# Kernel optimization log

Hardware: AMD Instinct MI355X
Metric: run time of the kernel (lower is better)

The kernel has to match this reference:

```python
import jax, jax.numpy as jnp
import numpy as np

N = 100000      # nodes
E = 2000000     # edges
F_NODE = 32     # num_node_features
F_EDGE = 16     # num_edge_features
HID = 128       # size_conv_layers
G = 4096        # num graphs (molecules)
NCLS = 2        # class_weights.shape[0]
NEG = 0.01      # LeakyReLU default negative slope
BN_EPS = 1e-5


def _bn(h, gamma, beta):
    # torch BatchNorm1d training-mode forward: biased batch stats over node dim
    m = jnp.mean(h, axis=0)
    v = jnp.var(h, axis=0)
    return (h - m) * jax.lax.rsqrt(v + BN_EPS) * gamma + beta


def _lrelu(h):
    return jnp.where(h > 0, h, NEG * h)


def setup_inputs() -> dict:
    key = jax.random.key(0)
    ks = jax.random.split(key, 64)
    d = {}
    d["x"] = jax.random.normal(ks[0], (N, F_NODE), dtype=jnp.float32)
    d["edge_index"] = jax.random.randint(ks[1], (2, E), 0, N, dtype=jnp.int64)
    d["edge_attr"] = jax.random.normal(ks[2], (E, F_EDGE), dtype=jnp.float32)
    d["batch"] = jnp.sort(jax.random.randint(ks[3], (N,), 0, G, dtype=jnp.int64))
    dims = [F_NODE, HID, HID]  # in_channels of each conv layer
    i = 4
    for l, ic in enumerate(dims):
        d[f"eps{l}"] = jnp.zeros((), jnp.float32)                                # GINE train_eps init 0
        d[f"ew{l}"] = 0.05 * jax.random.normal(ks[i], (F_EDGE, ic), jnp.float32); i += 1
        d[f"eb{l}"] = jnp.zeros((ic,), jnp.float32)
        d[f"w1{l}"] = 0.05 * jax.random.normal(ks[i], (ic, HID), jnp.float32); i += 1
        d[f"b1{l}"] = jnp.zeros((HID,), jnp.float32)
        d[f"g1{l}"] = jnp.ones((HID,), jnp.float32)
        d[f"be1{l}"] = jnp.zeros((HID,), jnp.float32)
        d[f"w2{l}"] = 0.05 * jax.random.normal(ks[i], (HID, HID), jnp.float32); i += 1
        d[f"b2{l}"] = jnp.zeros((HID,), jnp.float32)
        d[f"g2{l}"] = jnp.ones((HID,), jnp.float32)
        d[f"be2{l}"] = jnp.zeros((HID,), jnp.float32)
    d["wf"] = 0.05 * jax.random.normal(ks[i], (2 * HID, NCLS), jnp.float32)
    d["bf"] = jnp.zeros((NCLS,), jnp.float32)
    return d


def _forward(x, edge_index, edge_attr, batch, layers, wf, bf):
    src = edge_index[0]  # x_j (messages flow source->target in PyG)
    dst = edge_index[1]  # x_i
    for (eps, ew, eb, w1, b1, g1, be1, w2, b2, g2, be2) in layers:
        e = edge_attr @ ew + eb                     # [E, in_ch]
        msg = jax.nn.relu(x[src] + e)               # GINE message
        agg = jax.ops.segment_sum(msg, dst, num_segments=N)
        h = (1.0 + eps) * x + agg                   # [N, in_ch]
        h = _lrelu(_bn(h @ w1 + b1, g1, be1))       # nn: Lin->BN->LeakyReLU
        h = h @ w2 + b2                             # nn: Lin
        x = _lrelu(_bn(h, g2, be2))                 # outer BN + LeakyReLU
    pool = jax.ops.segment_sum(x, batch, num_segments=G)  # global_add_pool
    x_cat = jnp.concatenate([x, pool[batch]], axis=1)      # repeat_interleave broadcast
    logits = x_cat @ wf + bf
    return jax.nn.softmax(logits, axis=1)


def reference(x, edge_index, edge_attr, batch,
              eps0, ew0, eb0, w10, b10, g10, be10, w20, b20, g20, be20,
              eps1, ew1, eb1, w11, b11, g11, be11, w21, b21, g21, be21,
              eps2, ew2, eb2, w12, b12, g12, be12, w22, b22, g22, be22,
              wf, bf):
    layers = [
        (eps0, ew0, eb0, w10, b10, g10, be10, w20, b20, g20, be20),
        (eps1, ew1, eb1, w11, b11, g11, be11, w21, b21, g21, be21),
        (eps2, ew2, eb2, w12, b12, g12, be12, w22, b22, g22, be22),
    ]
    return _forward(x, edge_index, edge_attr, batch, layers, wf, bf)
```

## Files before the change

kernel.cpp:

```cpp
#include <hip/hip_runtime.h>

#define GEMM_GRID 512
#define GNUM 4096

typedef __attribute__((ext_vector_type(8))) short short8_t;
typedef __attribute__((ext_vector_type(4))) float f32x4;

__device__ __forceinline__ float bf2f(unsigned short u) {
    union { unsigned int i; float f; } v; v.i = ((unsigned int)u) << 16; return v.f;
}
__device__ __forceinline__ unsigned short f2bf(float f) {
    union { float f; unsigned int i; } v; v.f = f;
    unsigned int b = v.i + 0x7FFFu + ((v.i >> 16) & 1u);
    return (unsigned short)(b >> 16);
}
__device__ __forceinline__ float lrelu(float v) { return v > 0.f ? v : 0.01f * v; }

__global__ __launch_bounds__(256) void hist_kernel(
    const int* __restrict__ dstv, int* __restrict__ cnt, int E)
{
    int i = blockIdx.x * 256 + threadIdx.x;
    if (i < E) atomicAdd(&cnt[dstv[i] + 1], 1);
}

__global__ __launch_bounds__(256) void scan_block_kernel(
    int* __restrict__ data, int* __restrict__ bsum, int n)
{
    __shared__ int s[256];
    int tid = threadIdx.x;
    int base = blockIdx.x * 1024 + tid * 4;
    int v[4]; int run = 0;
    #pragma unroll
    for (int i = 0; i < 4; i++) {
        int x = (base + i < n) ? data[base + i] : 0;
        run += x; v[i] = run;
    }
    s[tid] = run; __syncthreads();
    for (int off = 1; off < 256; off <<= 1) {
        int t = (tid >= off) ? s[tid - off] : 0;
        __syncthreads();
        s[tid] += t;
        __syncthreads();
    }
    int excl = s[tid] - run;
    #pragma unroll
    for (int i = 0; i < 4; i++)
        if (base + i < n) data[base + i] = v[i] + excl;
    if (tid == 255) bsum[blockIdx.x] = s[255];
}

__global__ __launch_bounds__(128) void scan_carry_kernel(int* __restrict__ bsum, int nb)
{
    __shared__ int s[128];
    int tid = threadIdx.x;
    int orig = (tid < nb) ? bsum[tid] : 0;
    s[tid] = orig; __syncthreads();
    for (int off = 1; off < 128; off <<= 1) {
        int t = (tid >= off) ? s[tid - off] : 0;
        __syncthreads();
        s[tid] += t;
        __syncthreads();
    }
    if (tid < nb) bsum[tid] = s[tid] - orig;
}

__global__ __launch_bounds__(256) void scan_add_kernel(
    int* __restrict__ data, const int* __restrict__ bsum,
    int* __restrict__ cursor, int n, int N)
{
    int i = blockIdx.x * 256 + threadIdx.x;
    if (i < n) {
        int v = data[i] + bsum[i >> 10];
        data[i] = v;
        if (i < N) cursor[i] = v;
    }
}

__global__ __launch_bounds__(256) void scatter_kernel(
    const int* __restrict__ dstv, int* __restrict__ cursor,
    int* __restrict__ perm, int E)
{
    int i = blockIdx.x * 256 + threadIdx.x;
    if (i < E) {
        int p = atomicAdd(&cursor[dstv[i]], 1);
        perm[p] = i;
    }
}

__global__ __launch_bounds__(256) void reorder_kernel(
    const float* __restrict__ ea, const int* __restrict__ srcv,
    const int* __restrict__ perm, float* __restrict__ eap,
    int* __restrict__ srcp, int E)
{
    int i = blockIdx.x * 256 + threadIdx.x;
    int p = i >> 2, q = i & 3;
    if (p >= E) return;
    int e = perm[p];
    float4 v = reinterpret_cast<const float4*>(ea)[e * 4 + q];
    reinterpret_cast<float4*>(eap)[p * 4 + q] = v;
    if (q == 0) srcp[p] = srcv[e];
}

template<bool RO>
__global__ __launch_bounds__(256) void gather_kernel32(
    const float* __restrict__ ea, const int* __restrict__ srcv,
    const int* __restrict__ perm, const int* __restrict__ off,
    const float* __restrict__ ew, const float* __restrict__ ebias,
    const float* __restrict__ epsp, const float* __restrict__ x,
    float* __restrict__ agg, int N)
{
    int lane = threadIdx.x & 63;
    int n = __builtin_amdgcn_readfirstlane((int)((blockIdx.x * 256 + threadIdx.x) >> 6));
    if (n >= N) return;
    const int h = lane >> 5;
    const int c = lane & 31;
    float ewr[16];
    #pragma unroll
    for (int k = 0; k < 16; k++) ewr[k] = ew[k * 32 + c];
    const float ebr = ebias[c];
    float acc = 0.f;
    const int p0 = off[n], end = off[n + 1];
    for (int p = p0; p < end; p += 4) {
        int pa = p + h, pb = p + 2 + h;
        bool va = pa < end, vb = pb < end;
        int ia = va ? pa : p;
        int ib = vb ? pb : p;
        int eA = RO ? ia : perm[ia];
        int eB = RO ? ib : perm[ib];
        int sa = srcv[eA], sb = srcv[eB];
        const float4* apA = reinterpret_cast<const float4*>(ea + (size_t)eA * 16);
        const float4* apB = reinterpret_cast<const float4*>(ea + (size_t)eB * 16);
        float av[16], bv[16];
        #pragma unroll
        for (int q = 0; q < 4; q++) {
            float4 t = apA[q]; av[4*q]=t.x; av[4*q+1]=t.y; av[4*q+2]=t.z; av[4*q+3]=t.w;
            float4 u = apB[q]; bv[4*q]=u.x; bv[4*q+1]=u.y; bv[4*q+2]=u.z; bv[4*q+3]=u.w;
        }
        float xa = x[(size_t)sa * 32 + c];
        float xb = x[(size_t)sb * 32 + c];
        float ua = ebr, ub = ebr;
        #pragma unroll
        for (int k = 0; k < 16; k++) {
            ua = fmaf(av[k], ewr[k], ua);
            ub = fmaf(bv[k], ewr[k], ub);
        }
        acc += va ? fmaxf(xa + ua, 0.f) : 0.f;
        acc += vb ? fmaxf(xb + ub, 0.f) : 0.f;
    }
    acc += __shfl_xor(acc, 32);
    if (lane < 32) {
        float s = 1.f + epsp[0];
        agg[(size_t)n * 32 + c] = fmaf(x[(size_t)n * 32 + c], s, acc);
    }
}

template<bool RO>
__global__ __launch_bounds__(256) void gather_kernel128_bn(
    const float* __restrict__ ea, const int* __restrict__ srcv,
    const int* __restrict__ perm, const int* __restrict__ off,
    const float* __restrict__ ew, const float* __restrict__ ebias,
    const float* __restrict__ epsp, const float* __restrict__ U,
    const float* __restrict__ stats, const float* __restrict__ g,
    const float* __restrict__ be, float invN,
    float* __restrict__ agg, int N)
{
    int lane = threadIdx.x & 63;
    int n = __builtin_amdgcn_readfirstlane((int)((blockIdx.x * 256 + threadIdx.x) >> 6));
    if (n >= N) return;
    const int c0 = lane * 2;
    float sc0, sh0, sc1, sh1;
    {
        float m0 = stats[c0] * invN;
        float v0 = fmaxf(stats[128 + c0] * invN - m0 * m0, 0.f);
        sc0 = g[c0] * rsqrtf(v0 + 1e-5f);
        sh0 = be[c0] - m0 * sc0;
        float m1 = stats[c0 + 1] * invN;
        float v1 = fmaxf(stats[128 + c0 + 1] * invN - m1 * m1, 0.f);
        sc1 = g[c0 + 1] * rsqrtf(v1 + 1e-5f);
        sh1 = be[c0 + 1] - m1 * sc1;
    }
    float ew0[16], ew1[16];
    #pragma unroll
    for (int k = 0; k < 16; k++) {
        float2 w = *reinterpret_cast<const float2*>(&ew[k * 128 + c0]);
        ew0[k] = w.x; ew1[k] = w.y;
    }
    const float eb0 = ebias[c0], eb1 = ebias[c0 + 1];
    float acc0 = 0.f, acc1 = 0.f;
    int p = off[n];
    const int end = off[n + 1];
    for (; p + 2 <= end; p += 2) {
        int e0 = RO ? p : perm[p];
        int e1 = RO ? (p + 1) : perm[p + 1];
        int s0 = srcv[e0], s1 = srcv[e1];
        const float4* ap0 = reinterpret_cast<const float4*>(ea + (size_t)e0 * 16);
        const float4* ap1 = reinterpret_cast<const float4*>(ea + (size_t)e1 * 16);
        float av[16], bv[16];
        #pragma unroll
        for (int q = 0; q < 4; q++) {
            float4 t = ap0[q]; av[4*q]=t.x; av[4*q+1]=t.y; av[4*q+2]=t.z; av[4*q+3]=t.w;
            float4 u = ap1[q]; bv[4*q]=u.x; bv[4*q+1]=u.y; bv[4*q+2]=u.z; bv[4*q+3]=u.w;
        }
        float2 xv0 = *reinterpret_cast<const float2*>(&U[(size_t)s0 * 128 + c0]);
        float2 xv1 = *reinterpret_cast<const float2*>(&U[(size_t)s1 * 128 + c0]);
        float x00 = lrelu(fmaf(xv0.x, sc0, sh0));
        float x01 = lrelu(fmaf(xv0.y, sc1, sh1));
        float x10 = lrelu(fmaf(xv1.x, sc0, sh0));
        float x11 = lrelu(fmaf(xv1.y, sc1, sh1));
        float u0 = eb0, u1 = eb1, w0 = eb0, w1 = eb1;
        #pragma unroll
        for (int k = 0; k < 16; k++) {
            u0 = fmaf(av[k], ew0[k], u0);
            u1 = fmaf(av[k], ew1[k], u1);
            w0 = fmaf(bv[k], ew0[k], w0);
            w1 = fmaf(bv[k], ew1[k], w1);
        }
        acc0 += fmaxf(x00 + u0, 0.f) + fmaxf(x10 + w0, 0.f);
        acc1 += fmaxf(x01 + u1, 0.f) + fmaxf(x11 + w1, 0.f);
    }
    if (p < end) {
        int e0 = RO ? p : perm[p];
        int s0 = srcv[e0];
        const float4* ap0 = reinterpret_cast<const float4*>(ea + (size_t)e0 * 16);
        float av[16];
        #pragma unroll
        for (int q = 0; q < 4; q++) {
            float4 t = ap0[q]; av[4*q]=t.x; av[4*q+1]=t.y; av[4*q+2]=t.z; av[4*q+3]=t.w;
        }
        float2 xv0 = *reinterpret_cast<const float2*>(&U[(size_t)s0 * 128 + c0]);
        float x00 = lrelu(fmaf(xv0.x, sc0, sh0));
        float x01 = lrelu(fmaf(xv0.y, sc1, sh1));
        float u0 = eb0, u1 = eb1;
        #pragma unroll
        for (int k = 0; k < 16; k++) {
            u0 = fmaf(av[k], ew0[k], u0);
            u1 = fmaf(av[k], ew1[k], u1);
        }
        acc0 += fmaxf(x00 + u0, 0.f);
        acc1 += fmaxf(x01 + u1, 0.f);
    }
    float2 xn = *reinterpret_cast<const float2*>(&U[(size_t)n * 128 + c0]);
    float xn0 = lrelu(fmaf(xn.x, sc0, sh0));
    float xn1 = lrelu(fmaf(xn.y, sc1, sh1));
    float s = 1.f + epsp[0];
    float2 o;
    o.x = fmaf(xn0, s, acc0);
    o.y = fmaf(xn1, s, acc1);
    *reinterpret_cast<float2*>(&agg[(size_t)n * 128 + c0]) = o;
}

template<int K, bool BN_IN>
__global__ __launch_bounds__(256, 3) void gemm_mfma_kernel(
    const float* __restrict__ A,
    const float* __restrict__ stats_in, const float* __restrict__ g,
    const float* __restrict__ be, float invN,
    const float* __restrict__ W, const float* __restrict__ bias,
    float* __restrict__ out, float* __restrict__ stats_out, int N, int ntiles)
{
    constexpr int PA = K + 8;
    __shared__ unsigned short As_hi[32 * PA];
    __shared__ unsigned short As_lo[32 * PA];
    __shared__ unsigned short Wt[128 * PA];
    __shared__ float scale_s[K];
    __shared__ float shift_s[K];
    const int tid = threadIdx.x;
    const int w = tid >> 6;
    const int lane = tid & 63;
    const int quad = lane >> 4;
    const int l16 = lane & 15;
    const int rbase = (w & 1) * 16;
    const int nbase = (w >> 1) * 4;

    for (int idx = tid; idx < K * 128; idx += 256) {
        int k = idx >> 7, nn = idx & 127;
        Wt[nn * PA + k] = f2bf(W[idx]);
    }
    if (BN_IN) {
        for (int i = tid; i < K; i += 256) {
            float m = stats_in[i] * invN;
            float va = fmaxf(stats_in[K + i] * invN - m * m, 0.f);
            float sc = g[i] * rsqrtf(va + 1e-5f);
            scale_s[i] = sc;
            shift_s[i] = be[i] - m * sc;
        }
    }
    float bcol[4];
    #pragma unroll
    for (int nt = 0; nt < 4; nt++) bcol[nt] = bias[(nbase + nt) * 16 + l16];
    float csum[4] = {0.f, 0.f, 0.f, 0.f}, csq[4] = {0.f, 0.f, 0.f, 0.f};

    constexpr int C8 = K / 8;

    for (int tile = blockIdx.x; tile < ntiles; tile += gridDim.x) {
        const int row0 = tile * 32;
        __syncthreads();
        for (int cid = tid; cid < 32 * C8; cid += 256) {
            int row = cid / C8, c8 = cid % C8;
            int r = row0 + row;
            float f[8];
            if (r < N) {
                float4 u0 = *reinterpret_cast<const float4*>(&A[(size_t)r * K + c8 * 8]);
                float4 u1 = *reinterpret_cast<const float4*>(&A[(size_t)r * K + c8 * 8 + 4]);
                f[0]=u0.x; f[1]=u0.y; f[2]=u0.z; f[3]=u0.w;
                f[4]=u1.x; f[5]=u1.y; f[6]=u1.z; f[7]=u1.w;
            } else {
                #pragma unroll
                for (int j = 0; j < 8; j++) f[j] = 0.f;
            }
            if (BN_IN) {
                int kb = c8 * 8;
                #pragma unroll
                for (int j = 0; j < 8; j++)
                    f[j] = lrelu(fmaf(f[j], scale_s[kb + j], shift_s[kb + j]));
            }
            unsigned int hi[4], lo[4];
            #pragma unroll
            for (int j = 0; j < 4; j++) {
                unsigned int b0 = __float_as_uint(f[2*j]);
                unsigned int b1 = __float_as_uint(f[2*j + 1]);
                hi[j] = __builtin_amdgcn_perm(b1, b0, 0x07060302u);
                float l0 = f[2*j]     - __uint_as_float(b0 & 0xffff0000u);
                float l1 = f[2*j + 1] - __uint_as_float(b1 & 0xffff0000u);
                lo[j] = __builtin_amdgcn_perm(__float_as_uint(l1), __float_as_uint(l0), 0x07060302u);
            }
            *reinterpret_cast<uint4*>(&As_hi[row * PA + c8 * 8]) = make_uint4(hi[0], hi[1], hi[2], hi[3]);
            *reinterpret_cast<uint4*>(&As_lo[row * PA + c8 * 8]) = make_uint4(lo[0], lo[1], lo[2], lo[3]);
        }
        __syncthreads();

        f32x4 acc[4];
        #pragma unroll
        for (int nt = 0; nt < 4; nt++) { f32x4 z = {0.f,0.f,0.f,0.f}; acc[nt] = z; }
        #pragma unroll
        for (int chunk = 0; chunk < K / 32; chunk++) {
            short8_t ahi = *reinterpret_cast<const short8_t*>(
                &As_hi[(rbase + l16) * PA + chunk * 32 + quad * 8]);
            short8_t alo = *reinterpret_cast<const short8_t*>(
                &As_lo[(rbase + l16) * PA + chunk * 32 + quad * 8]);
            #pragma unroll
            for (int nt = 0; nt < 4; nt++) {
                short8_t bfr = *reinterpret_cast<const short8_t*>(
                    &Wt[((nbase + nt) * 16 + l16) * PA + chunk * 32 + quad * 8]);
                acc[nt] = __builtin_amdgcn_mfma_f32_16x16x32_bf16(alo, bfr, acc[nt], 0, 0, 0);
                acc[nt] = __builtin_amdgcn_mfma_f32_16x16x32_bf16(ahi, bfr, acc[nt], 0, 0, 0);
            }
        }
        const int rb = row0 + rbase + quad * 4;
        #pragma unroll
        for (int nt = 0; nt < 4; nt++) {
            #pragma unroll
            for (int rg = 0; rg < 4; rg++) {
                int r = rb + rg;
                if (r < N) {
                    float v = acc[nt][rg] + bcol[nt];
                    out[(size_t)r * 128 + (nbase + nt) * 16 + l16] = v;
                    csum[nt] += v; csq[nt] += v * v;
                }
            }
        }
    }
    #pragma unroll
    for (int nt = 0; nt < 4; nt++) {
        float s = csum[nt]; s += __shfl_xor(s, 16); s += __shfl_xor(s, 32);
        float q = csq[nt];  q += __shfl_xor(q, 16); q += __shfl_xor(q, 32);
        if (quad == 0) {
            int col = (nbase + nt) * 16 + l16;
            atomicAdd(&stats_out[col], s);
            atomicAdd(&stats_out[128 + col], q);
        }
    }
}

__global__ __launch_bounds__(256) void pool_kernel_bn(
    const float* __restrict__ U, const int* __restrict__ batch,
    const float* __restrict__ stats, const float* __restrict__ g,
    const float* __restrict__ be, float invN,
    float* __restrict__ pool, int N)
{
    int w = (blockIdx.x * 256 + threadIdx.x) >> 6;
    int lane = threadIdx.x & 63;
    int n0 = w * 32;
    if (n0 >= N) return;
    int n1 = min(n0 + 32, N);
    int c0 = lane * 2;
    float sc0, sh0, sc1, sh1;
    {
        float m0 = stats[c0] * invN;
        float v0 = fmaxf(stats[128 + c0] * invN - m0 * m0, 0.f);
        sc0 = g[c0] * rsqrtf(v0 + 1e-5f);
        sh0 = be[c0] - m0 * sc0;
        float m1 = stats[c0 + 1] * invN;
        float v1 = fmaxf(stats[128 + c0 + 1] * invN - m1 * m1, 0.f);
        sc1 = g[c0 + 1] * rsqrtf(v1 + 1e-5f);
        sh1 = be[c0 + 1] - m1 * sc1;
    }
    float a0 = 0.f, a1 = 0.f;
    int cur = batch[n0];
    for (int n = n0; n < n1; ++n) {
        int b = batch[n];
        if (b != cur) {
            atomicAdd(&pool[(size_t)cur * 128 + c0], a0);
            atomicAdd(&pool[(size_t)cur * 128 + c0 + 1], a1);
            a0 = a1 = 0.f; cur = b;
        }
        float2 v = *reinterpret_cast<const float2*>(&U[(size_t)n * 128 + c0]);
        a0 += lrelu(fmaf(v.x, sc0, sh0));
        a1 += lrelu(fmaf(v.y, sc1, sh1));
    }
    atomicAdd(&pool[(size_t)cur * 128 + c0], a0);
    atomicAdd(&pool[(size_t)cur * 128 + c0 + 1], a1);
}

__global__ __launch_bounds__(256) void final_kernel_bn(
    const float* __restrict__ U, const float* __restrict__ pool,
    const int* __restrict__ batch,
    const float* __restrict__ stats, const float* __restrict__ g,
    const float* __restrict__ be, float invN,
    const float* __restrict__ wf, const float* __restrict__ bf,
    float* __restrict__ out, int N)
{
    __shared__ float wf_s[512];
    int tid = threadIdx.x;
    for (int i = tid; i < 512; i += 256) wf_s[i] = wf[i];
    __syncthreads();
    int wid = tid >> 6, lane = tid & 63;
    int n = blockIdx.x * 4 + wid;
    if (n >= N) return;
    int cA = lane, cB = 64 + lane;
    float scA, shA, scB, shB;
    {
        float mA = stats[cA] * invN;
        float vA = fmaxf(stats[128 + cA] * invN - mA * mA, 0.f);
        scA = g[cA] * rsqrtf(vA + 1e-5f);
        shA = be[cA] - mA * scA;
        float mB = stats[cB] * invN;
        float vB = fmaxf(stats[128 + cB] * invN - mB * mB, 0.f);
        scB = g[cB] * rsqrtf(vB + 1e-5f);
        shB = be[cB] - mB * scB;
    }
    int b = batch[n];
    float v0 = lrelu(fmaf(U[(size_t)n * 128 + cA], scA, shA));
    float v1 = lrelu(fmaf(U[(size_t)n * 128 + cB], scB, shB));
    float p0 = pool[(size_t)b * 128 + cA];
    float p1 = pool[(size_t)b * 128 + cB];
    float a0 = v0 * wf_s[lane * 2]       + v1 * wf_s[(64 + lane) * 2]
             + p0 * wf_s[(128 + lane) * 2] + p1 * wf_s[(192 + lane) * 2];
    float a1 = v0 * wf_s[lane * 2 + 1]       + v1 * wf_s[(64 + lane) * 2 + 1]
             + p0 * wf_s[(128 + lane) * 2 + 1] + p1 * wf_s[(192 + lane) * 2 + 1];
    #pragma unroll
    for (int off = 32; off >= 1; off >>= 1) {
        a0 += __shfl_down(a0, off);
        a1 += __shfl_down(a1, off);
    }
    if (lane == 0) {
        a0 += bf[0]; a1 += bf[1];
        float mx = fmaxf(a0, a1);
        float e0 = __expf(a0 - mx), e1 = __expf(a1 - mx);
        float inv = 1.f / (e0 + e1);
        out[(size_t)n * 2]     = e0 * inv;
        out[(size_t)n * 2 + 1] = e1 * inv;
    }
}

extern "C" void kernel_launch(void* const* d_in, const int* in_sizes, int n_in,
                              void* d_out, int out_size, void* d_ws, size_t ws_size,
                              hipStream_t stream)
{
    const float* x0    = (const float*)d_in[0];
    const int*   ei    = (const int*)d_in[1];
    const float* ea    = (const float*)d_in[2];
    const int*   batch = (const int*)d_in[3];
    const int E = in_sizes[1] / 2;
    const int N = in_sizes[3];
    const int* srcv = ei;
    const int* dstv = ei + E;
    const float* wf = (const float*)d_in[37];
    const float* bfp = (const float*)d_in[38];
    float* out = (float*)d_out;
    const float invN = 1.0f / (float)N;
    const int ntiles = (N + 31) / 32;

    const size_t base_f = (size_t)2 * N * 128 + (size_t)GNUM * 128 + 6 * 256
                        + (size_t)(N + 1) + (size_t)N + 128 + (size_t)E;
    const size_t full_f = base_f + (size_t)E * 16 + (size_t)E;
    const bool ro = (ws_size >= full_f * 4);

    float* ws = (float*)d_ws;
    size_t o = 0;
    float* xA    = ws + o; o += (size_t)N * 128;
    float* xB    = ws + o; o += (size_t)N * 128;
    float* eap   = ws + o; o += ro ? (size_t)E * 16 : 0;
    float* poolb = ws + o; o += (size_t)GNUM * 128;
    float* statsb= ws + o; o += 6 * 256;
    int* srcp    = (int*)(ws + o); o += ro ? (size_t)E : 0;
    int* off     = (int*)(ws + o); o += (size_t)(N + 1);
    int* cursor  = (int*)(ws + o); o += (size_t)N;
    int* bsumb   = (int*)(ws + o); o += 128;
    int* perm    = (int*)(ws + o);

    hipMemsetAsync(off, 0, (size_t)(N + 1) * sizeof(int), stream);
    hipMemsetAsync(statsb, 0, (size_t)6 * 256 * sizeof(float), stream);
    hipMemsetAsync(poolb, 0, (size_t)GNUM * 128 * sizeof(float), stream);
    hist_kernel<<<(E + 255) / 256, 256, 0, stream>>>(dstv, off, E);
    const int n1 = N + 1;
    const int nb = (n1 + 1023) / 1024;
    scan_block_kernel<<<nb, 256, 0, stream>>>(off, bsumb, n1);
    scan_carry_kernel<<<1, 128, 0, stream>>>(bsumb, nb);
    scan_add_kernel<<<(n1 + 255) / 256, 256, 0, stream>>>(off, bsumb, cursor, n1, N);
    scatter_kernel<<<(E + 255) / 256, 256, 0, stream>>>(dstv, cursor, perm, E);
    if (ro)
        reorder_kernel<<<(E * 4 + 255) / 256, 256, 0, stream>>>(ea, srcv, perm, eap, srcp, E);

    const float* g_ea  = ro ? eap  : ea;
    const int*   g_src = ro ? srcp : srcv;
    const int gather_blocks = (N + 3) / 4;

    float* Uprev = nullptr;
    const float *pg = nullptr, *pbe = nullptr;
    float* pstats = nullptr;

    for (int l = 0; l < 3; l++) {
        const int C = (l == 0) ? 32 : 128;
        int bidx = 4 + l * 11;
        const float* epsp = (const float*)d_in[bidx + 0];
        const float* ew   = (const float*)d_in[bidx + 1];
        const float* eb   = (const float*)d_in[bidx + 2];
        const float* w1   = (const float*)d_in[bidx + 3];
        const float* b1   = (const float*)d_in[bidx + 4];
        const float* g1   = (const float*)d_in[bidx + 5];
        const float* be1  = (const float*)d_in[bidx + 6];
        const float* w2   = (const float*)d_in[bidx + 7];
        const float* b2   = (const float*)d_in[bidx + 8];
        const float* g2   = (const float*)d_in[bidx + 9];
        const float* be2  = (const float*)d_in[bidx + 10];
        float* st1 = statsb + (size_t)(l * 2) * 256;
        float* st2 = statsb + (size_t)(l * 2 + 1) * 256;

        if (l == 0) {
            if (ro) gather_kernel32<true><<<gather_blocks, 256, 0, stream>>>(
                        g_ea, g_src, perm, off, ew, eb, epsp, x0, xB, N);
            else    gather_kernel32<false><<<gather_blocks, 256, 0, stream>>>(
                        g_ea, g_src, perm, off, ew, eb, epsp, x0, xB, N);
            gemm_mfma_kernel<32, false><<<GEMM_GRID, 256, 0, stream>>>(
                xB, nullptr, nullptr, nullptr, invN, w1, b1, xA, st1, N, ntiles);
            gemm_mfma_kernel<128, true><<<GEMM_GRID, 256, 0, stream>>>(
                xA, st1, g1, be1, invN, w2, b2, xA, st2, N, ntiles);
            Uprev = xA;
        } else {
            float* dst = (Uprev == xA) ? xB : xA;
            if (ro) gather_kernel128_bn<true><<<gather_blocks, 256, 0, stream>>>(
                        g_ea, g_src, perm, off, ew, eb, epsp, Uprev,
                        pstats, pg, pbe, invN, dst, N);
            else    gather_kernel128_bn<false><<<gather_blocks, 256, 0, stream>>>(
                        g_ea, g_src, perm, off, ew, eb, epsp, Uprev,
                        pstats, pg, pbe, invN, dst, N);
            gemm_mfma_kernel<128, false><<<GEMM_GRID, 256, 0, stream>>>(
                dst, nullptr, nullptr, nullptr, invN, w1, b1, dst, st1, N, ntiles);
            gemm_mfma_kernel<128, true><<<GEMM_GRID, 256, 0, stream>>>(
                dst, st1, g1, be1, invN, w2, b2, dst, st2, N, ntiles);
            Uprev = dst;
        }
        pstats = st2; pg = g2; pbe = be2;
    }
    pool_kernel_bn<<<((N + 31) / 32 * 64 + 255) / 256, 256, 0, stream>>>(
        Uprev, batch, pstats, pg, pbe, invN, poolb, N);
    final_kernel_bn<<<(N + 3) / 4, 256, 0, stream>>>(
        Uprev, poolb, batch, pstats, pg, pbe, invN, wf, bfp, out, N);
}
```

Baseline: 1.487 ms.

## Emit aggregation as split bf16 hi/lo planes consumed directly by first GEMM

```diff
diff --git a/kernel.cpp b/kernel.cpp
--- a/kernel.cpp
+++ b/kernel.cpp
@@ -5,6 +5,7 @@
 
 typedef __attribute__((ext_vector_type(8))) short short8_t;
 typedef __attribute__((ext_vector_type(4))) float f32x4;
+typedef __attribute__((ext_vector_type(2))) float v2f;
 
 __device__ __forceinline__ float bf2f(unsigned short u) {
     union { unsigned int i; float f; } v; v.i = ((unsigned int)u) << 16; return v.f;
@@ -107,7 +108,7 @@
     const int* __restrict__ perm, const int* __restrict__ off,
     const float* __restrict__ ew, const float* __restrict__ ebias,
     const float* __restrict__ epsp, const float* __restrict__ x,
-    float* __restrict__ agg, int N)
+    unsigned short* __restrict__ aggh, unsigned short* __restrict__ aggl, int N)
 {
     int lane = threadIdx.x & 63;
     int n = __builtin_amdgcn_readfirstlane((int)((blockIdx.x * 256 + threadIdx.x) >> 6));
@@ -150,7 +151,12 @@
     acc += __shfl_xor(acc, 32);
     if (lane < 32) {
         float s = 1.f + epsp[0];
-        agg[(size_t)n * 32 + c] = fmaf(x[(size_t)n * 32 + c], s, acc);
+        float f = fmaf(x[(size_t)n * 32 + c], s, acc);
+        unsigned int b = __float_as_uint(f);
+        unsigned short hi = (unsigned short)(b >> 16);
+        float lo = f - __uint_as_float(b & 0xffff0000u);
+        aggh[(size_t)n * 32 + c] = hi;
+        aggl[(size_t)n * 32 + c] = f2bf(lo);
     }
 }
 
@@ -162,31 +168,29 @@
     const float* __restrict__ epsp, const float* __restrict__ U,
     const float* __restrict__ stats, const float* __restrict__ g,
     const float* __restrict__ be, float invN,
-    float* __restrict__ agg, int N)
+    unsigned short* __restrict__ aggh, unsigned short* __restrict__ aggl, int N)
 {
     int lane = threadIdx.x & 63;
     int n = __builtin_amdgcn_readfirstlane((int)((blockIdx.x * 256 + threadIdx.x) >> 6));
     if (n >= N) return;
     const int c0 = lane * 2;
-    float sc0, sh0, sc1, sh1;
+    v2f scv, shv;
     {
         float m0 = stats[c0] * invN;
         float v0 = fmaxf(stats[128 + c0] * invN - m0 * m0, 0.f);
-        sc0 = g[c0] * rsqrtf(v0 + 1e-5f);
-        sh0 = be[c0] - m0 * sc0;
+        scv.x = g[c0] * rsqrtf(v0 + 1e-5f);
+        shv.x = be[c0] - m0 * scv.x;
         float m1 = stats[c0 + 1] * invN;
         float v1 = fmaxf(stats[128 + c0 + 1] * invN - m1 * m1, 0.f);
-        sc1 = g[c0 + 1] * rsqrtf(v1 + 1e-5f);
-        sh1 = be[c0 + 1] - m1 * sc1;
-    }
-    float ew0[16], ew1[16];
-    #pragma unroll
-    for (int k = 0; k < 16; k++) {
-        float2 w = *reinterpret_cast<const float2*>(&ew[k * 128 + c0]);
-        ew0[k] = w.x; ew1[k] = w.y;
-    }
-    const float eb0 = ebias[c0], eb1 = ebias[c0 + 1];
-    float acc0 = 0.f, acc1 = 0.f;
+        scv.y = g[c0 + 1] * rsqrtf(v1 + 1e-5f);
+        shv.y = be[c0 + 1] - m1 * scv.y;
+    }
+    v2f ewv[16];
+    #pragma unroll
+    for (int k = 0; k < 16; k++)
+        ewv[k] = *reinterpret_cast<const v2f*>(&ew[k * 128 + c0]);
+    const v2f ebv = *reinterpret_cast<const v2f*>(&ebias[c0]);
+    v2f acc = {0.f, 0.f};
     int p = off[n];
     const int end = off[n + 1];
     for (; p + 2 <= end; p += 2) {
@@ -201,22 +205,22 @@
             float4 t = ap0[q]; av[4*q]=t.x; av[4*q+1]=t.y; av[4*q+2]=t.z; av[4*q+3]=t.w;
             float4 u = ap1[q]; bv[4*q]=u.x; bv[4*q+1]=u.y; bv[4*q+2]=u.z; bv[4*q+3]=u.w;
         }
-        float2 xv0 = *reinterpret_cast<const float2*>(&U[(size_t)s0 * 128 + c0]);
-        float2 xv1 = *reinterpret_cast<const float2*>(&U[(size_t)s1 * 128 + c0]);
-        float x00 = lrelu(fmaf(xv0.x, sc0, sh0));
-        float x01 = lrelu(fmaf(xv0.y, sc1, sh1));
-        float x10 = lrelu(fmaf(xv1.x, sc0, sh0));
-        float x11 = lrelu(fmaf(xv1.y, sc1, sh1));
-        float u0 = eb0, u1 = eb1, w0 = eb0, w1 = eb1;
+        v2f xv0 = *reinterpret_cast<const v2f*>(&U[(size_t)s0 * 128 + c0]);
+        v2f xv1 = *reinterpret_cast<const v2f*>(&U[(size_t)s1 * 128 + c0]);
+        v2f x0b = xv0 * scv + shv;
+        v2f x1b = xv1 * scv + shv;
+        x0b.x = lrelu(x0b.x); x0b.y = lrelu(x0b.y);
+        x1b.x = lrelu(x1b.x); x1b.y = lrelu(x1b.y);
+        v2f u = ebv, w = ebv;
         #pragma unroll
         for (int k = 0; k < 16; k++) {
-            u0 = fmaf(av[k], ew0[k], u0);
-            u1 = fmaf(av[k], ew1[k], u1);
-            w0 = fmaf(bv[k], ew0[k], w0);
-            w1 = fmaf(bv[k], ew1[k], w1);
-        }
-        acc0 += fmaxf(x00 + u0, 0.f) + fmaxf(x10 + w0, 0.f);
-        acc1 += fmaxf(x01 + u1, 0.f) + fmaxf(x11 + w1, 0.f);
+            u = ewv[k] * av[k] + u;
+            w = ewv[k] * bv[k] + w;
+        }
+        v2f m0 = x0b + u, m1 = x1b + w;
+        m0.x = fmaxf(m0.x, 0.f); m0.y = fmaxf(m0.y, 0.f);
+        m1.x = fmaxf(m1.x, 0.f); m1.y = fmaxf(m1.y, 0.f);
+        acc = acc + m0 + m1;
     }
     if (p < end) {
         int e0 = RO ? p : perm[p];
@@ -227,36 +231,130 @@
         for (int q = 0; q < 4; q++) {
             float4 t = ap0[q]; av[4*q]=t.x; av[4*q+1]=t.y; av[4*q+2]=t.z; av[4*q+3]=t.w;
         }
-        float2 xv0 = *reinterpret_cast<const float2*>(&U[(size_t)s0 * 128 + c0]);
-        float x00 = lrelu(fmaf(xv0.x, sc0, sh0));
-        float x01 = lrelu(fmaf(xv0.y, sc1, sh1));
-        float u0 = eb0, u1 = eb1;
-        #pragma unroll
-        for (int k = 0; k < 16; k++) {
-            u0 = fmaf(av[k], ew0[k], u0);
-            u1 = fmaf(av[k], ew1[k], u1);
-        }
-        acc0 += fmaxf(x00 + u0, 0.f);
-        acc1 += fmaxf(x01 + u1, 0.f);
-    }
-    float2 xn = *reinterpret_cast<const float2*>(&U[(size_t)n * 128 + c0]);
-    float xn0 = lrelu(fmaf(xn.x, sc0, sh0));
-    float xn1 = lrelu(fmaf(xn.y, sc1, sh1));
+        v2f xv0 = *reinterpret_cast<const v2f*>(&U[(size_t)s0 * 128 + c0]);
+        v2f x0b = xv0 * scv + shv;
+        x0b.x = lrelu(x0b.x); x0b.y = lrelu(x0b.y);
+        v2f u = ebv;
+        #pragma unroll
+        for (int k = 0; k < 16; k++) u = ewv[k] * av[k] + u;
+        v2f m0 = x0b + u;
+        m0.x = fmaxf(m0.x, 0.f); m0.y = fmaxf(m0.y, 0.f);
+        acc = acc + m0;
+    }
+    v2f xn = *reinterpret_cast<const v2f*>(&U[(size_t)n * 128 + c0]);
+    v2f xnb = xn * scv + shv;
+    xnb.x = lrelu(xnb.x); xnb.y = lrelu(xnb.y);
     float s = 1.f + epsp[0];
-    float2 o;
-    o.x = fmaf(xn0, s, acc0);
-    o.y = fmaf(xn1, s, acc1);
-    *reinterpret_cast<float2*>(&agg[(size_t)n * 128 + c0]) = o;
-}
-
-template<int K, bool BN_IN>
-__global__ __launch_bounds__(256, 3) void gemm_mfma_kernel(
+    v2f o = xnb * s + acc;
+    unsigned int b0 = __float_as_uint(o.x);
+    unsigned int b1 = __float_as_uint(o.y);
+    unsigned int hp = __builtin_amdgcn_perm(b1, b0, 0x07060302u);
+    float l0 = o.x - __uint_as_float(b0 & 0xffff0000u);
+    float l1 = o.y - __uint_as_float(b1 & 0xffff0000u);
+    unsigned int lp = (unsigned int)f2bf(l0) | ((unsigned int)f2bf(l1) << 16);
+    *reinterpret_cast<unsigned int*>(&aggh[(size_t)n * 128 + c0]) = hp;
+    *reinterpret_cast<unsigned int*>(&aggl[(size_t)n * 128 + c0]) = lp;
+}
+
+template<int K>
+__global__ __launch_bounds__(256, 3) void gemm_copy_mfma_kernel(
+    const unsigned short* __restrict__ Ah, const unsigned short* __restrict__ Al,
+    const float* __restrict__ W, const float* __restrict__ bias,
+    float* __restrict__ out, float* __restrict__ stats_out, int N, int ntiles)
+{
+    constexpr int PA = K + 8;
+    __shared__ unsigned short As_hi[32 * PA];
+    __shared__ unsigned short As_lo[32 * PA];
+    __shared__ unsigned short Wt[128 * PA];
+    const int tid = threadIdx.x;
+    const int w = tid >> 6;
+    const int lane = tid & 63;
+    const int quad = lane >> 4;
+    const int l16 = lane & 15;
+    const int rbase = (w & 1) * 16;
+    const int nbase = (w >> 1) * 4;
+
+    for (int idx = tid; idx < K * 128; idx += 256) {
+        int k = idx >> 7, nn = idx & 127;
+        Wt[nn * PA + k] = f2bf(W[idx]);
+    }
+    float bcol[4];
+    #pragma unroll
+    for (int nt = 0; nt < 4; nt++) bcol[nt] = bias[(nbase + nt) * 16 + l16];
+    float csum[4] = {0.f, 0.f, 0.f, 0.f}, csq[4] = {0.f, 0.f, 0.f, 0.f};
+
+    constexpr int C8 = K / 8;
+
+    for (int tile = blockIdx.x; tile < ntiles; tile += gridDim.x) {
+        const int row0 = tile * 32;
+        __syncthreads();
+        for (int cid = tid; cid < 32 * C8; cid += 256) {
+            int row = cid / C8, c8 = cid % C8;
+            int r = row0 + row;
+            uint4 h, l;
+            if (r < N) {
+                h = *reinterpret_cast<const uint4*>(&Ah[(size_t)r * K + c8 * 8]);
+                l = *reinterpret_cast<const uint4*>(&Al[(size_t)r * K + c8 * 8]);
+            } else {
+                h = make_uint4(0u,0u,0u,0u);
+                l = make_uint4(0u,0u,0u,0u);
+            }
+            *reinterpret_cast<uint4*>(&As_hi[row * PA + c8 * 8]) = h;
+            *reinterpret_cast<uint4*>(&As_lo[row * PA + c8 * 8]) = l;
+        }
+        __syncthreads();
+
+        f32x4 acc[4];
+        #pragma unroll
+        for (int nt = 0; nt < 4; nt++) { f32x4 z = {0.f,0.f,0.f,0.f}; acc[nt] = z; }
+        #pragma unroll
+        for (int chunk = 0; chunk < K / 32; chunk++) {
+            short8_t ahi = *reinterpret_cast<const short8_t*>(
+                &As_hi[(rbase + l16) * PA + chunk * 32 + quad * 8]);
+            short8_t alo = *reinterpret_cast<const short8_t*>(
+                &As_lo[(rbase + l16) * PA + chunk * 32 + quad * 8]);
+            #pragma unroll
+            for (int nt = 0; nt < 4; nt++) {
+                short8_t bfr = *reinterpret_cast<const short8_t*>(
+                    &Wt[((nbase + nt) * 16 + l16) * PA + chunk * 32 + quad * 8]);
+                acc[nt] = __builtin_amdgcn_mfma_f32_16x16x32_bf16(alo, bfr, acc[nt], 0, 0, 0);
+                acc[nt] = __builtin_amdgcn_mfma_f32_16x16x32_bf16(ahi, bfr, acc[nt], 0, 0, 0);
+            }
+        }
+        const int rb = row0 + rbase + quad * 4;
+        #pragma unroll
+        for (int nt = 0; nt < 4; nt++) {
+            #pragma unroll
+            for (int rg = 0; rg < 4; rg++) {
+                int r = rb + rg;
+                if (r < N) {
+                    float v = acc[nt][rg] + bcol[nt];
+                    out[(size_t)r * 128 + (nbase + nt) * 16 + l16] = v;
+                    csum[nt] += v; csq[nt] += v * v;
+                }
+            }
+        }
+    }
+    #pragma unroll
+    for (int nt = 0; nt < 4; nt++) {
+        float s = csum[nt]; s += __shfl_xor(s, 16); s += __shfl_xor(s, 32);
+        float q = csq[nt];  q += __shfl_xor(q, 16); q += __shfl_xor(q, 32);
+        if (quad == 0) {
+            int col = (nbase + nt) * 16 + l16;
+            atomicAdd(&stats_out[col], s);
+            atomicAdd(&stats_out[128 + col], q);
+        }
+    }
+}
+
+__global__ __launch_bounds__(256, 3) void gemm_bn_mfma_kernel(
     const float* __restrict__ A,
     const float* __restrict__ stats_in, const float* __restrict__ g,
     const float* __restrict__ be, float invN,
     const float* __restrict__ W, const float* __restrict__ bias,
     float* __restrict__ out, float* __restrict__ stats_out, int N, int ntiles)
 {
+    constexpr int K = 128;
     constexpr int PA = K + 8;
     __shared__ unsigned short As_hi[32 * PA];
     __shared__ unsigned short As_lo[32 * PA];
@@ -275,14 +373,12 @@
         int k = idx >> 7, nn = idx & 127;
         Wt[nn * PA + k] = f2bf(W[idx]);
     }
-    if (BN_IN) {
-        for (int i = tid; i < K; i += 256) {
-            float m = stats_in[i] * invN;
-            float va = fmaxf(stats_in[K + i] * invN - m * m, 0.f);
-            float sc = g[i] * rsqrtf(va + 1e-5f);
-            scale_s[i] = sc;
-            shift_s[i] = be[i] - m * sc;
-        }
+    for (int i = tid; i < K; i += 256) {
+        float m = stats_in[i] * invN;
+        float va = fmaxf(stats_in[K + i] * invN - m * m, 0.f);
+        float sc = g[i] * rsqrtf(va + 1e-5f);
+        scale_s[i] = sc;
+        shift_s[i] = be[i] - m * sc;
     }
     float bcol[4];
     #pragma unroll
@@ -307,12 +403,10 @@
                 #pragma unroll
                 for (int j = 0; j < 8; j++) f[j] = 0.f;
             }
-            if (BN_IN) {
-                int kb = c8 * 8;
-                #pragma unroll
-                for (int j = 0; j < 8; j++)
-                    f[j] = lrelu(fmaf(f[j], scale_s[kb + j], shift_s[kb + j]));
-            }
+            int kb = c8 * 8;
+            #pragma unroll
+            for (int j = 0; j < 8; j++)
+                f[j] = lrelu(fmaf(f[j], scale_s[kb + j], shift_s[kb + j]));
             unsigned int hi[4], lo[4];
             #pragma unroll
             for (int j = 0; j < 4; j++) {
@@ -498,6 +592,8 @@
     int* bsumb   = (int*)(ws + o); o += 128;
     int* perm    = (int*)(ws + o);
 
+    unsigned short* planeh = (unsigned short*)xB;
+
     hipMemsetAsync(off, 0, (size_t)(N + 1) * sizeof(int), stream);
     hipMemsetAsync(statsb, 0, (size_t)6 * 256 * sizeof(float), stream);
     hipMemsetAsync(poolb, 0, (size_t)GNUM * 128 * sizeof(float), stream);
@@ -515,7 +611,6 @@
     const int*   g_src = ro ? srcp : srcv;
     const int gather_blocks = (N + 3) / 4;
 
-    float* Uprev = nullptr;
     const float *pg = nullptr, *pbe = nullptr;
     float* pstats = nullptr;
 
@@ -536,34 +631,32 @@
         float* st1 = statsb + (size_t)(l * 2) * 256;
         float* st2 = statsb + (size_t)(l * 2 + 1) * 256;
 
+        unsigned short* ah = planeh;
+        unsigned short* al = planeh + (size_t)N * C;
+
         if (l == 0) {
             if (ro) gather_kernel32<true><<<gather_blocks, 256, 0, stream>>>(
-                        g_ea, g_src, perm, off, ew, eb, epsp, x0, xB, N);
+                        g_ea, g_src, perm, off, ew, eb, epsp, x0, ah, al, N);
             else    gather_kernel32<false><<<gather_blocks, 256, 0, stream>>>(
-                        g_ea, g_src, perm, off, ew, eb, epsp, x0, xB, N);
-            gemm_mfma_kernel<32, false><<<GEMM_GRID, 256, 0, stream>>>(
-                xB, nullptr, nullptr, nullptr, invN, w1, b1, xA, st1, N, ntiles);
-            gemm_mfma_kernel<128, true><<<GEMM_GRID, 256, 0, stream>>>(
-                xA, st1, g1, be1, invN, w2, b2, xA, st2, N, ntiles);
-            Uprev = xA;
+                        g_ea, g_src, perm, off, ew, eb, epsp, x0, ah, al, N);
+            gemm_copy_mfma_kernel<32><<<GEMM_GRID, 256, 0, stream>>>(
+                ah, al, w1, b1, xA, st1, N, ntiles);
         } else {
-            float* dst = (Uprev == xA) ? xB : xA;
             if (ro) gather_kernel128_bn<true><<<gather_blocks, 256, 0, stream>>>(
-                        g_ea, g_src, perm, off, ew, eb, epsp, Uprev,
-                        pstats, pg, pbe, invN, dst, N);
+                        g_ea, g_src, perm, off, ew, eb, epsp, xA,
+                        pstats, pg, pbe, invN, ah, al, N);
             else    gather_kernel128_bn<false><<<gather_blocks, 256, 0, stream>>>(
-                        g_ea, g_src, perm, off, ew, eb, epsp, Uprev,
-                        pstats, pg, pbe, invN, dst, N);
-            gemm_mfma_kernel<128, false><<<GEMM_GRID, 256, 0, stream>>>(
-                dst, nullptr, nullptr, nullptr, invN, w1, b1, dst, st1, N, ntiles);
-            gemm_mfma_kernel<128, true><<<GEMM_GRID, 256, 0, stream>>>(
-                dst, st1, g1, be1, invN, w2, b2, dst, st2, N, ntiles);
-            Uprev = dst;
-        }
+                        g_ea, g_src, perm, off, ew, eb, epsp, xA,
+                        pstats, pg, pbe, invN, ah, al, N);
+            gemm_copy_mfma_kernel<128><<<GEMM_GRID, 256, 0, stream>>>(
+                ah, al, w1, b1, xA, st1, N, ntiles);
+        }
+        gemm_bn_mfma_kernel<<<GEMM_GRID, 256, 0, stream>>>(
+            xA, st1, g1, be1, invN, w2, b2, xA, st2, N, ntiles);
         pstats = st2; pg = g2; pbe = be2;
     }
     pool_kernel_bn<<<((N + 31) / 32 * 64 + 255) / 256, 256, 0, stream>>>(
-        Uprev, batch, pstats, pg, pbe, invN, poolb, N);
+        xA, batch, pstats, pg, pbe, invN, poolb, N);
     final_kernel_bn<<<(N + 3) / 4, 256, 0, stream>>>(
-        Uprev, poolb, batch, pstats, pg, pbe, invN, wf, bfp, out, N);
-}
+        xA, poolb, batch, pstats, pg, pbe, invN, wf, bfp, out, N);
+}
```

New measurement: 1.458 ms. Within noise of the previous version (-1.9%).
